# Performance work log

Hardware: AMD Instinct MI355X
Metric: run time of the kernel (lower is better)

## Reference

```python
import jax, jax.numpy as jnp
import numpy as np

B, T, D_ENC, H, NUM_CLASSES = 256, 256, 512, 512, 96


def setup_inputs() -> dict:
    key = jax.random.key(0)
    ks = jax.random.split(key, 12)
    s = lambda k, shp, fan: jax.random.normal(k, shp, jnp.float32) / np.sqrt(fan)
    return {
        "prev_h": jax.random.normal(ks[0], (B, H), jnp.float32),
        "prev_c": jax.random.normal(ks[1], (B, H), jnp.float32),
        "batch_H": jax.random.normal(ks[2], (B, T, D_ENC), jnp.float32),
        "char_onehots": jax.random.uniform(ks[3], (B, NUM_CLASSES), jnp.float32),
        # i2h: Dense(D_ENC -> H, no bias); h2h: Dense(H -> H, bias); score: Dense(H -> 1, no bias)
        "Wi2h": s(ks[4], (D_ENC, H), D_ENC),
        "Wh2h": s(ks[5], (H, H), H),
        "bh2h": jnp.zeros((H,), jnp.float32),
        "Wscore": s(ks[6], (H, 1), H),
        # LSTMCell: input dim = D_ENC + NUM_CLASSES, gates [i, f, g, o]
        "Wk": s(ks[7], (D_ENC + NUM_CLASSES, 4 * H), D_ENC + NUM_CLASSES),
        "Uk": s(ks[8], (H, 4 * H), H),
        "bk": jnp.zeros((4 * H,), jnp.float32),
    }


def reference(prev_h, prev_c, batch_H, char_onehots, Wi2h, Wh2h, bh2h, Wscore, Wk, Uk, bk):
    # Bahdanau additive attention
    bH_proj = jnp.einsum('btd,dh->bth', batch_H, Wi2h)          # [B,T,H]
    h_proj = (prev_h @ Wh2h + bh2h)[:, None, :]                  # [B,1,H]
    e = jnp.tanh(bH_proj + h_proj) @ Wscore                      # [B,T,1]
    alpha = jax.nn.softmax(e, axis=1)                            # [B,T,1]
    context = jnp.einsum('bt,btd->bd', alpha[..., 0], batch_H)   # [B,D_enc]
    # LSTM cell step on [context ; char_onehots]
    x = jnp.concatenate([context, char_onehots], axis=1)         # [B, D_enc+num_classes]
    z = x @ Wk + prev_h @ Uk + bk                                # [B, 4H]
    i, f, g, o = jnp.split(z, 4, axis=1)
    c_new = jax.nn.sigmoid(f) * prev_c + jax.nn.sigmoid(i) * jnp.tanh(g)
    h_new = jax.nn.sigmoid(o) * jnp.tanh(c_new)
    return h_new, c_new, alpha
```

## Files before the change

kernel.cpp:

```cpp
#include <hip/hip_runtime.h>

typedef __bf16 bf16_t;
typedef bf16_t bf16x8 __attribute__((ext_vector_type(8)));
typedef unsigned short ushort8_t __attribute__((ext_vector_type(8)));
typedef unsigned short ushort4_t __attribute__((ext_vector_type(4)));
typedef float f32x4 __attribute__((ext_vector_type(4)));

__device__ __forceinline__ unsigned short f2bf(float f) {
    __bf16 h = (__bf16)f;
    return __builtin_bit_cast(unsigned short, h);
}
__device__ __forceinline__ float fast_tanh(float x) {
    float e2 = __expf(2.f * x);
    return 1.f - 2.f / (e2 + 1.f);
}
__device__ __forceinline__ float fast_sig(float x) {
    return 1.f / (1.f + __expf(-x));
}

__global__ void k0_wt2(const float* __restrict__ Wi2h, const float* __restrict__ Wh2h,
                       unsigned short* __restrict__ Wt, unsigned short* __restrict__ Wht) {
    __shared__ float tile[32][33];
    const float* W = blockIdx.z ? Wh2h : Wi2h;
    unsigned short* O = blockIdx.z ? Wht : Wt;
    int tx = threadIdx.x, ty = threadIdx.y;
    int bx = blockIdx.x, by = blockIdx.y;
#pragma unroll
    for (int j = 0; j < 4; ++j) {
        int r = by * 32 + ty + j * 8;
        int c = bx * 32 + tx;
        tile[ty + j * 8][tx] = W[r * 512 + c];
    }
    __syncthreads();
#pragma unroll
    for (int j = 0; j < 4; ++j) {
        int h = bx * 32 + ty + j * 8;
        int d = by * 32 + tx;
        O[h * 512 + d] = f2bf(tile[tx][ty + j * 8]);
    }
}

__global__ void k1x_conv(const float* __restrict__ src, unsigned short* __restrict__ dst) {
    int i = blockIdx.x * 256 + threadIdx.x;
    float4 f = ((const float4*)src)[i];
    ushort4_t u;
    u[0] = f2bf(f.x); u[1] = f2bf(f.y); u[2] = f2bf(f.z); u[3] = f2bf(f.w);
    ((ushort4_t*)dst)[i] = u;
}

__global__ void k1m_hproj(const unsigned short* __restrict__ ph_bf,
                          const unsigned short* __restrict__ Wht,
                          const float* __restrict__ bh2h,
                          float* __restrict__ h_proj) {
    int tid = threadIdx.x;
    int wave = tid >> 6, lane = tid & 63;
    int l15 = lane & 15, g = lane >> 4;
    int h0 = blockIdx.x * 64 + wave * 16;
    int m0 = blockIdx.y * 32;

    f32x4 acc[2];
    acc[0] = (f32x4){0.f, 0.f, 0.f, 0.f};
    acc[1] = (f32x4){0.f, 0.f, 0.f, 0.f};

    const unsigned short* abase = ph_bf + (size_t)(m0 + l15) * 512 + g * 8;
    const unsigned short* bbase = Wht + (size_t)(h0 + l15) * 512 + g * 8;
#pragma unroll
    for (int j = 0; j < 16; ++j) {
        bf16x8 bf = __builtin_bit_cast(bf16x8, *(const ushort8_t*)(bbase + j * 32));
        bf16x8 a0 = __builtin_bit_cast(bf16x8, *(const ushort8_t*)(abase + j * 32));
        bf16x8 a1 = __builtin_bit_cast(bf16x8, *(const ushort8_t*)(abase + 16 * 512 + j * 32));
        acc[0] = __builtin_amdgcn_mfma_f32_16x16x32_bf16(a0, bf, acc[0], 0, 0, 0);
        acc[1] = __builtin_amdgcn_mfma_f32_16x16x32_bf16(a1, bf, acc[1], 0, 0, 0);
    }
    int h = h0 + l15;
    float bias = bh2h[h];
#pragma unroll
    for (int mf = 0; mf < 2; ++mf)
#pragma unroll
        for (int r = 0; r < 4; ++r)
            h_proj[(size_t)(m0 + mf * 16 + g * 4 + r) * 512 + h] = acc[mf][r] + bias;
}

__launch_bounds__(256, 1)
__global__ void k2v4_scores(const float* __restrict__ batch_H,
                            const unsigned short* __restrict__ Wt,
                            const float* __restrict__ h_proj,
                            const float* __restrict__ Wscore,
                            float* __restrict__ e_out) {
    __shared__ __align__(16) unsigned short Asw[128 * 512];
    __shared__ float hp_s[512];
    __shared__ float wsc_s[512];
    __shared__ float e_red[4][64];

    int tid = threadIdx.x;
    int m0  = blockIdx.x * 128;
    int b   = m0 >> 8;

    hp_s[tid]        = h_proj[(size_t)b * 512 + tid];
    hp_s[tid + 256]  = h_proj[(size_t)b * 512 + tid + 256];
    wsc_s[tid]       = Wscore[tid];
    wsc_s[tid + 256] = Wscore[tid + 256];

    {
        int dr = tid >> 4;
        int cc = tid & 15;
#pragma unroll
        for (int j = 0; j < 32; ++j) {
            int r = (j >> 2) * 16 + dr;
            int c = (j & 3) * 16 + cc;
            const float* src = batch_H + (size_t)(m0 + r) * 512 + c * 8;
            float4 f0 = *(const float4*)(src);
            float4 f1 = *(const float4*)(src + 4);
            ushort8_t u;
            u[0] = f2bf(f0.x); u[1] = f2bf(f0.y); u[2] = f2bf(f0.z); u[3] = f2bf(f0.w);
            u[4] = f2bf(f1.x); u[5] = f2bf(f1.y); u[6] = f2bf(f1.z); u[7] = f2bf(f1.w);
            *(ushort8_t*)((char*)Asw + r * 1024 + ((c ^ (r & 7)) << 4)) = u;
        }
    }
    __syncthreads();

    int wave = tid >> 6;
    int lane = tid & 63;
    int wr = wave >> 1;
    int wc = wave & 1;
    int l15 = lane & 15, g = lane >> 4;

    float s[4][4];
#pragma unroll
    for (int mf = 0; mf < 4; ++mf)
#pragma unroll
        for (int r = 0; r < 4; ++r) s[mf][r] = 0.f;

    const unsigned short* wtb = Wt + (size_t)(wc * 64 + l15) * 512 + g * 8;

    for (int nc = 0; nc < 4; ++nc) {
        f32x4 acc[4][4];
#pragma unroll
        for (int mf = 0; mf < 4; ++mf)
#pragma unroll
            for (int nf = 0; nf < 4; ++nf)
                acc[mf][nf] = (f32x4){0.f, 0.f, 0.f, 0.f};

        const unsigned short* wnc = wtb + (size_t)nc * 128 * 512;

        bf16x8 bq[4][4];
#pragma unroll
        for (int ks0 = 0; ks0 < 4; ++ks0)
#pragma unroll
            for (int nf = 0; nf < 4; ++nf)
                bq[ks0][nf] = __builtin_bit_cast(bf16x8,
                    *(const ushort8_t*)(wnc + (size_t)nf * 16 * 512 + ks0 * 32));

#pragma unroll
        for (int ks = 0; ks < 16; ++ks) {
            bf16x8 af[4];
#pragma unroll
            for (int mf = 0; mf < 4; ++mf) {
                int row = wr * 64 + mf * 16 + l15;
                af[mf] = __builtin_bit_cast(bf16x8,
                    *(const ushort8_t*)((char*)Asw + row * 1024 + (((ks * 4 + g) ^ (row & 7)) << 4)));
            }
#pragma unroll
            for (int nf = 0; nf < 4; ++nf)
#pragma unroll
                for (int mf = 0; mf < 4; ++mf)
                    acc[mf][nf] = __builtin_amdgcn_mfma_f32_16x16x32_bf16(
                        af[mf], bq[ks & 3][nf], acc[mf][nf], 0, 0, 0);
            if (ks < 12) {
#pragma unroll
                for (int nf = 0; nf < 4; ++nf)
                    bq[ks & 3][nf] = __builtin_bit_cast(bf16x8,
                        *(const ushort8_t*)(wnc + (size_t)nf * 16 * 512 + (ks + 4) * 32));
            }
        }

#pragma unroll
        for (int nf = 0; nf < 4; ++nf) {
            int nl = nc * 128 + wc * 64 + nf * 16 + l15;
            float hpv = hp_s[nl], wv = wsc_s[nl];
#pragma unroll
            for (int mf = 0; mf < 4; ++mf)
#pragma unroll
                for (int r = 0; r < 4; ++r)
                    s[mf][r] += wv * fast_tanh(acc[mf][nf][r] + hpv);
        }
    }

#pragma unroll
    for (int mf = 0; mf < 4; ++mf)
#pragma unroll
        for (int r = 0; r < 4; ++r) {
            float v = s[mf][r];
            v += __shfl_xor(v, 1);
            v += __shfl_xor(v, 2);
            v += __shfl_xor(v, 4);
            v += __shfl_xor(v, 8);
            s[mf][r] = v;
        }
    if (l15 == 0) {
#pragma unroll
        for (int mf = 0; mf < 4; ++mf)
#pragma unroll
            for (int r = 0; r < 4; ++r)
                e_red[wave][mf * 16 + g * 4 + r] = s[mf][r];
    }
    __syncthreads();
    if (tid < 128) {
        int wrr = tid >> 6, rl = tid & 63;
        e_out[m0 + wrr * 64 + rl] = e_red[wrr * 2 + 0][rl] + e_red[wrr * 2 + 1][rl];
    }
}

__global__ void k3_softmax(const float* __restrict__ e, float* __restrict__ alpha_out) {
    __shared__ float red[4];
    int b = blockIdx.x, tid = threadIdx.x;
    float v = e[b * 256 + tid];
    float mx = v;
#pragma unroll
    for (int off = 32; off; off >>= 1) mx = fmaxf(mx, __shfl_xor(mx, off));
    if ((tid & 63) == 0) red[tid >> 6] = mx;
    __syncthreads();
    mx = fmaxf(fmaxf(red[0], red[1]), fmaxf(red[2], red[3]));
    float p = __expf(v - mx);
    __syncthreads();
    float sum = p;
#pragma unroll
    for (int off = 32; off; off >>= 1) sum += __shfl_xor(sum, off);
    if ((tid & 63) == 0) red[tid >> 6] = sum;
    __syncthreads();
    sum = red[0] + red[1] + red[2] + red[3];
    alpha_out[b * 256 + tid] = p / sum;
}

__global__ void k4_context(const float* __restrict__ batch_H, const float* __restrict__ alpha,
                           float* __restrict__ context) {
    __shared__ float al[256];
    int b = blockIdx.y, dc = blockIdx.x, tid = threadIdx.x;
    al[tid] = alpha[b * 256 + tid];
    __syncthreads();
    int d = dc * 256 + tid;
    const float* bh = batch_H + (size_t)b * 256 * 512 + d;
    float acc = 0.f;
#pragma unroll 4
    for (int t = 0; t < 256; ++t)
        acc += al[t] * bh[(size_t)t * 512];
    context[b * 512 + d] = acc;
}

__global__ void k5t_wzt(const float* __restrict__ Wk, const float* __restrict__ Uk,
                        unsigned short* __restrict__ Wzt) {
    __shared__ float tile[32][33];
    int tx = threadIdx.x, ty = threadIdx.y;
    int bx = blockIdx.x;
    int by = blockIdx.y;
#pragma unroll
    for (int j = 0; j < 4; ++j) {
        int k = bx * 32 + ty + j * 8;
        int c = by * 32 + tx;
        float v = (k < 608) ? Wk[(size_t)k * 2048 + c] : Uk[(size_t)(k - 608) * 2048 + c];
        tile[ty + j * 8][tx] = v;
    }
    __syncthreads();
#pragma unroll
    for (int j = 0; j < 4; ++j) {
        int n = by * 32 + ty + j * 8;
        int k = bx * 32 + tx;
        Wzt[(size_t)n * 1120 + k] = f2bf(tile[tx][ty + j * 8]);
    }
}

__global__ void k5x_build(const float* __restrict__ context, const float* __restrict__ onehots,
                          const float* __restrict__ prev_h, unsigned short* __restrict__ xb) {
    int b = blockIdx.x, tid = threadIdx.x;
    for (int k = tid; k < 1120; k += 256) {
        float v;
        if (k < 512)      v = context[b * 512 + k];
        else if (k < 608) v = onehots[b * 96 + k - 512];
        else              v = prev_h[b * 512 + k - 608];
        xb[(size_t)b * 1120 + k] = f2bf(v);
    }
}

__launch_bounds__(256)
__global__ void k5m_fused(const unsigned short* __restrict__ xb,
                          const unsigned short* __restrict__ Wzt,
                          const float* __restrict__ bk,
                          const float* __restrict__ prev_c,
                          float* __restrict__ out) {
    __shared__ __align__(16) unsigned short Axs[32 * 232];

    int tid  = threadIdx.x;
    int wave = tid >> 6;
    int lane = tid & 63;
    int l15  = lane & 15;
    int g    = lane >> 4;
    int b0   = blockIdx.y * 32;
    int h0   = blockIdx.x * 64 + wave * 16;

    f32x4 acc[2][4];
#pragma unroll
    for (int mf = 0; mf < 2; ++mf)
#pragma unroll
        for (int gt = 0; gt < 4; ++gt)
            acc[mf][gt] = (f32x4){0.f, 0.f, 0.f, 0.f};

    const unsigned short* wbase = Wzt + (size_t)(h0 + l15) * 1120;

    for (int ks = 0; ks < 5; ++ks) {
        if (ks) __syncthreads();
        int kbase = ks * 224;
        for (int i = tid; i < 896; i += 256) {
            int row = i / 28;
            int c8  = (i % 28) * 8;
            *(ushort8_t*)(&Axs[row * 232 + c8]) =
                *(const ushort8_t*)(&xb[(size_t)(b0 + row) * 1120 + kbase + c8]);
        }
        __syncthreads();

        bf16x8 bcur[4], bnxt[4];
#pragma unroll
        for (int gt = 0; gt < 4; ++gt)
            bcur[gt] = __builtin_bit_cast(bf16x8,
                *(const ushort8_t*)(wbase + (size_t)gt * 512 * 1120 + kbase + g * 8));

#pragma unroll
        for (int kb = 0; kb < 7; ++kb) {
            if (kb < 6) {
                int kg = kbase + (kb + 1) * 32 + g * 8;
#pragma unroll
                for (int gt = 0; gt < 4; ++gt)
                    bnxt[gt] = __builtin_bit_cast(bf16x8,
                        *(const ushort8_t*)(wbase + (size_t)gt * 512 * 1120 + kg));
            }
            bf16x8 afrag[2];
#pragma unroll
            for (int mf = 0; mf < 2; ++mf)
                afrag[mf] = __builtin_bit_cast(bf16x8,
                    *(const ushort8_t*)(&Axs[(mf * 16 + l15) * 232 + kb * 32 + g * 8]));
#pragma unroll
            for (int gt = 0; gt < 4; ++gt)
#pragma unroll
                for (int mf = 0; mf < 2; ++mf)
                    acc[mf][gt] = __builtin_amdgcn_mfma_f32_16x16x32_bf16(
                        afrag[mf], bcur[gt], acc[mf][gt], 0, 0, 0);
#pragma unroll
            for (int gt = 0; gt < 4; ++gt) bcur[gt] = bnxt[gt];
        }
    }

    int h = h0 + l15;
    float bi = bk[h], bfv = bk[512 + h], bg = bk[1024 + h], bo = bk[1536 + h];
#pragma unroll
    for (int mf = 0; mf < 2; ++mf)
#pragma unroll
        for (int r = 0; r < 4; ++r) {
            int m = b0 + mf * 16 + g * 4 + r;
            float zi = acc[mf][0][r] + bi;
            float zf = acc[mf][1][r] + bfv;
            float zg = acc[mf][2][r] + bg;
            float zo = acc[mf][3][r] + bo;
            float c  = fast_sig(zf) * prev_c[m * 512 + h] + fast_sig(zi) * fast_tanh(zg);
            float hn = fast_sig(zo) * fast_tanh(c);
            out[m * 512 + h]          = hn;
            out[131072 + m * 512 + h] = c;
        }
}

extern "C" void kernel_launch(void* const* d_in, const int* in_sizes, int n_in,
                              void* d_out, int out_size, void* d_ws, size_t ws_size,
                              hipStream_t stream) {
    (void)in_sizes; (void)n_in; (void)out_size; (void)ws_size;
    const float* prev_h  = (const float*)d_in[0];
    const float* prev_c  = (const float*)d_in[1];
    const float* batch_H = (const float*)d_in[2];
    const float* onehots = (const float*)d_in[3];
    const float* Wi2h    = (const float*)d_in[4];
    const float* Wh2h    = (const float*)d_in[5];
    const float* bh2h    = (const float*)d_in[6];
    const float* Wscore  = (const float*)d_in[7];
    const float* Wk      = (const float*)d_in[8];
    const float* Uk      = (const float*)d_in[9];
    const float* bk      = (const float*)d_in[10];
    float* out = (float*)d_out;
    float* alpha = out + 262144;

    char* ws = (char*)d_ws;
    unsigned short* Wt     = (unsigned short*)(ws + 0);
    unsigned short* Wht    = (unsigned short*)(ws + 524288);
    unsigned short* ph_bf  = (unsigned short*)(ws + 1048576);
    float*          h_proj = (float*)(ws + 1310720);
    float*          e      = (float*)(ws + 1835008);
    unsigned short* Wzt    = (unsigned short*)(ws + 0);
    unsigned short* xb     = (unsigned short*)(ws + 4587520);
    float*          context= (float*)(ws + 5160960);

    k0_wt2     <<<dim3(16, 16, 2), dim3(32, 8), 0, stream>>>(Wi2h, Wh2h, Wt, Wht);
    k1x_conv   <<<128, 256, 0, stream>>>(prev_h, ph_bf);
    k1m_hproj  <<<dim3(8, 8), 256, 0, stream>>>(ph_bf, Wht, bh2h, h_proj);
    k2v4_scores<<<512, 256, 0, stream>>>(batch_H, Wt, h_proj, Wscore, e);
    k3_softmax <<<256, 256, 0, stream>>>(e, alpha);
    k4_context <<<dim3(2, 256), 256, 0, stream>>>(batch_H, alpha, context);
    k5t_wzt    <<<dim3(35, 64), dim3(32, 8), 0, stream>>>(Wk, Uk, Wzt);
    k5x_build  <<<256, 256, 0, stream>>>(context, onehots, prev_h, xb);
    k5m_fused  <<<dim3(8, 8), 256, 0, stream>>>(xb, Wzt, bk, prev_c, out);
}
```

Before: 177.5 us.

## Restructure attention scores kernel with LDS-resident weight tile and streamed activations

```diff
diff --git a/kernel.cpp b/kernel.cpp
--- a/kernel.cpp
+++ b/kernel.cpp
@@ -81,140 +81,155 @@
             h_proj[(size_t)(m0 + mf * 16 + g * 4 + r) * 512 + h] = acc[mf][r] + bias;
 }
 
-__launch_bounds__(256, 1)
-__global__ void k2v4_scores(const float* __restrict__ batch_H,
+__launch_bounds__(512, 1)
+__global__ void k2v5_scores(const float* __restrict__ batch_H,
                             const unsigned short* __restrict__ Wt,
                             const float* __restrict__ h_proj,
                             const float* __restrict__ Wscore,
-                            float* __restrict__ e_out) {
-    __shared__ __align__(16) unsigned short Asw[128 * 512];
-    __shared__ float hp_s[512];
-    __shared__ float wsc_s[512];
-    __shared__ float e_red[4][64];
-
-    int tid = threadIdx.x;
-    int m0  = blockIdx.x * 128;
-    int b   = m0 >> 8;
-
-    hp_s[tid]        = h_proj[(size_t)b * 512 + tid];
-    hp_s[tid + 256]  = h_proj[(size_t)b * 512 + tid + 256];
-    wsc_s[tid]       = Wscore[tid];
-    wsc_s[tid + 256] = Wscore[tid + 256];
-
-    {
-        int dr = tid >> 4;
-        int cc = tid & 15;
-#pragma unroll
-        for (int j = 0; j < 32; ++j) {
-            int r = (j >> 2) * 16 + dr;
-            int c = (j & 3) * 16 + cc;
-            const float* src = batch_H + (size_t)(m0 + r) * 512 + c * 8;
-            float4 f0 = *(const float4*)(src);
-            float4 f1 = *(const float4*)(src + 4);
-            ushort8_t u;
-            u[0] = f2bf(f0.x); u[1] = f2bf(f0.y); u[2] = f2bf(f0.z); u[3] = f2bf(f0.w);
-            u[4] = f2bf(f1.x); u[5] = f2bf(f1.y); u[6] = f2bf(f1.z); u[7] = f2bf(f1.w);
-            *(ushort8_t*)((char*)Asw + r * 1024 + ((c ^ (r & 7)) << 4)) = u;
-        }
-    }
-    __syncthreads();
-
+                            float* __restrict__ e_part8) {
+    __shared__ __align__(16) char Bsw[128 * 1024];
+
+    int tid  = threadIdx.x;
     int wave = tid >> 6;
     int lane = tid & 63;
-    int wr = wave >> 1;
-    int wc = wave & 1;
-    int l15 = lane & 15, g = lane >> 4;
-
-    float s[4][4];
-#pragma unroll
-    for (int mf = 0; mf < 4; ++mf)
-#pragma unroll
-        for (int r = 0; r < 4; ++r) s[mf][r] = 0.f;
-
-    const unsigned short* wtb = Wt + (size_t)(wc * 64 + l15) * 512 + g * 8;
-
-    for (int nc = 0; nc < 4; ++nc) {
-        f32x4 acc[4][4];
-#pragma unroll
-        for (int mf = 0; mf < 4; ++mf)
+    int l15  = lane & 15, g = lane >> 4;
+    int wr   = wave >> 1;
+    int wc   = wave & 1;
+
+    int xcd = blockIdx.x & 7, j = blockIdx.x >> 3;
+    int mgroup = xcd * 8 + (j >> 2);
+    int nt = j & 3;
+    int n0 = nt * 128;
+
+#pragma unroll
+    for (int i = 0; i < 16; ++i) {
+        int row = i * 8 + wave;
+        int chS = lane ^ (row & 7);
+        const unsigned short* src = Wt + (size_t)(n0 + row) * 512 + chS * 8;
+        __builtin_amdgcn_global_load_lds(
+            (const __attribute__((address_space(1))) void*)src,
+            (__attribute__((address_space(3))) void*)(Bsw + row * 1024), 16, 0, 0);
+    }
+    __syncthreads();
+
+    float wv[4];
+#pragma unroll
+    for (int nf = 0; nf < 4; ++nf)
+        wv[nf] = Wscore[n0 + wc * 64 + nf * 16 + l15];
+
+    int slot = nt * 2 + wc;
+
+    float4 pf[2][2][2];
+
+    {
+        int m00 = mgroup * 1024;
+#pragma unroll
+        for (int ks = 0; ks < 2; ++ks)
+#pragma unroll
+            for (int mf = 0; mf < 2; ++mf) {
+                const float* ap = batch_H + (size_t)(m00 + wr * 32 + mf * 16 + l15) * 512 + ks * 32 + g * 8;
+                pf[ks][mf][0] = *(const float4*)(ap);
+                pf[ks][mf][1] = *(const float4*)(ap + 4);
+            }
+    }
+
+    for (int p = 0; p < 8; ++p) {
+        int m0 = (mgroup * 8 + p) * 128;
+        int b  = (mgroup * 8 + p) >> 1;
+
+        float hp[4];
+#pragma unroll
+        for (int nf = 0; nf < 4; ++nf)
+            hp[nf] = h_proj[(size_t)b * 512 + n0 + wc * 64 + nf * 16 + l15];
+
+        f32x4 acc[2][4];
+#pragma unroll
+        for (int mf = 0; mf < 2; ++mf)
 #pragma unroll
             for (int nf = 0; nf < 4; ++nf)
                 acc[mf][nf] = (f32x4){0.f, 0.f, 0.f, 0.f};
 
-        const unsigned short* wnc = wtb + (size_t)nc * 128 * 512;
-
-        bf16x8 bq[4][4];
-#pragma unroll
-        for (int ks0 = 0; ks0 < 4; ++ks0)
-#pragma unroll
-            for (int nf = 0; nf < 4; ++nf)
-                bq[ks0][nf] = __builtin_bit_cast(bf16x8,
-                    *(const ushort8_t*)(wnc + (size_t)nf * 16 * 512 + ks0 * 32));
-
 #pragma unroll
         for (int ks = 0; ks < 16; ++ks) {
-            bf16x8 af[4];
-#pragma unroll
-            for (int mf = 0; mf < 4; ++mf) {
-                int row = wr * 64 + mf * 16 + l15;
-                af[mf] = __builtin_bit_cast(bf16x8,
-                    *(const ushort8_t*)((char*)Asw + row * 1024 + (((ks * 4 + g) ^ (row & 7)) << 4)));
-            }
-#pragma unroll
-            for (int nf = 0; nf < 4; ++nf)
-#pragma unroll
-                for (int mf = 0; mf < 4; ++mf)
+            const int par = ks & 1;
+            bf16x8 af[2];
+#pragma unroll
+            for (int mf = 0; mf < 2; ++mf) {
+                ushort8_t u;
+                u[0] = f2bf(pf[par][mf][0].x); u[1] = f2bf(pf[par][mf][0].y);
+                u[2] = f2bf(pf[par][mf][0].z); u[3] = f2bf(pf[par][mf][0].w);
+                u[4] = f2bf(pf[par][mf][1].x); u[5] = f2bf(pf[par][mf][1].y);
+                u[6] = f2bf(pf[par][mf][1].z); u[7] = f2bf(pf[par][mf][1].w);
+                af[mf] = __builtin_bit_cast(bf16x8, u);
+            }
+            if (ks < 14) {
+#pragma unroll
+                for (int mf = 0; mf < 2; ++mf) {
+                    const float* ap = batch_H + (size_t)(m0 + wr * 32 + mf * 16 + l15) * 512 + (ks + 2) * 32 + g * 8;
+                    pf[par][mf][0] = *(const float4*)(ap);
+                    pf[par][mf][1] = *(const float4*)(ap + 4);
+                }
+            } else if (p < 7) {
+#pragma unroll
+                for (int mf = 0; mf < 2; ++mf) {
+                    const float* ap = batch_H + (size_t)(m0 + 128 + wr * 32 + mf * 16 + l15) * 512 + (ks - 14) * 32 + g * 8;
+                    pf[par][mf][0] = *(const float4*)(ap);
+                    pf[par][mf][1] = *(const float4*)(ap + 4);
+                }
+            }
+#pragma unroll
+            for (int nf = 0; nf < 4; ++nf) {
+                int brow = wc * 64 + nf * 16 + l15;
+                bf16x8 bfv = __builtin_bit_cast(bf16x8,
+                    *(const ushort8_t*)(Bsw + brow * 1024 + (((ks * 4 + g) ^ (brow & 7)) << 4)));
+#pragma unroll
+                for (int mf = 0; mf < 2; ++mf)
                     acc[mf][nf] = __builtin_amdgcn_mfma_f32_16x16x32_bf16(
-                        af[mf], bq[ks & 3][nf], acc[mf][nf], 0, 0, 0);
-            if (ks < 12) {
-#pragma unroll
-                for (int nf = 0; nf < 4; ++nf)
-                    bq[ks & 3][nf] = __builtin_bit_cast(bf16x8,
-                        *(const ushort8_t*)(wnc + (size_t)nf * 16 * 512 + (ks + 4) * 32));
-            }
-        }
-
+                        af[mf], bfv, acc[mf][nf], 0, 0, 0);
+            }
+        }
+
+        float s[2][4];
+#pragma unroll
+        for (int mf = 0; mf < 2; ++mf)
+#pragma unroll
+            for (int r = 0; r < 4; ++r) s[mf][r] = 0.f;
 #pragma unroll
         for (int nf = 0; nf < 4; ++nf) {
-            int nl = nc * 128 + wc * 64 + nf * 16 + l15;
-            float hpv = hp_s[nl], wv = wsc_s[nl];
-#pragma unroll
-            for (int mf = 0; mf < 4; ++mf)
+#pragma unroll
+            for (int mf = 0; mf < 2; ++mf)
 #pragma unroll
                 for (int r = 0; r < 4; ++r)
-                    s[mf][r] += wv * fast_tanh(acc[mf][nf][r] + hpv);
-        }
-    }
-
-#pragma unroll
-    for (int mf = 0; mf < 4; ++mf)
-#pragma unroll
-        for (int r = 0; r < 4; ++r) {
-            float v = s[mf][r];
-            v += __shfl_xor(v, 1);
-            v += __shfl_xor(v, 2);
-            v += __shfl_xor(v, 4);
-            v += __shfl_xor(v, 8);
-            s[mf][r] = v;
-        }
-    if (l15 == 0) {
-#pragma unroll
-        for (int mf = 0; mf < 4; ++mf)
-#pragma unroll
-            for (int r = 0; r < 4; ++r)
-                e_red[wave][mf * 16 + g * 4 + r] = s[mf][r];
-    }
-    __syncthreads();
-    if (tid < 128) {
-        int wrr = tid >> 6, rl = tid & 63;
-        e_out[m0 + wrr * 64 + rl] = e_red[wrr * 2 + 0][rl] + e_red[wrr * 2 + 1][rl];
-    }
-}
-
-__global__ void k3_softmax(const float* __restrict__ e, float* __restrict__ alpha_out) {
+                    s[mf][r] += wv[nf] * fast_tanh(acc[mf][nf][r] + hp[nf]);
+        }
+#pragma unroll
+        for (int mf = 0; mf < 2; ++mf)
+#pragma unroll
+            for (int r = 0; r < 4; ++r) {
+                float v = s[mf][r];
+                v += __shfl_xor(v, 1);
+                v += __shfl_xor(v, 2);
+                v += __shfl_xor(v, 4);
+                v += __shfl_xor(v, 8);
+                s[mf][r] = v;
+            }
+        if (l15 == 0) {
+#pragma unroll
+            for (int mf = 0; mf < 2; ++mf) {
+                f32x4 o = (f32x4){s[mf][0], s[mf][1], s[mf][2], s[mf][3]};
+                *(f32x4*)(e_part8 + (size_t)slot * 65536 + m0 + wr * 32 + mf * 16 + g * 4) = o;
+            }
+        }
+    }
+}
+
+__global__ void k3_softmax(const float* __restrict__ e_part8, float* __restrict__ alpha_out) {
     __shared__ float red[4];
     int b = blockIdx.x, tid = threadIdx.x;
-    float v = e[b * 256 + tid];
+    int m = b * 256 + tid;
+    float v = 0.f;
+#pragma unroll
+    for (int s = 0; s < 8; ++s) v += e_part8[(size_t)s * 65536 + m];
     float mx = v;
 #pragma unroll
     for (int off = 32; off; off >>= 1) mx = fmaxf(mx, __shfl_xor(mx, off));
@@ -385,20 +400,20 @@
     float* alpha = out + 262144;
 
     char* ws = (char*)d_ws;
-    unsigned short* Wt     = (unsigned short*)(ws + 0);
-    unsigned short* Wht    = (unsigned short*)(ws + 524288);
-    unsigned short* ph_bf  = (unsigned short*)(ws + 1048576);
-    float*          h_proj = (float*)(ws + 1310720);
-    float*          e      = (float*)(ws + 1835008);
-    unsigned short* Wzt    = (unsigned short*)(ws + 0);
-    unsigned short* xb     = (unsigned short*)(ws + 4587520);
-    float*          context= (float*)(ws + 5160960);
+    unsigned short* Wt      = (unsigned short*)(ws + 0);
+    unsigned short* Wht     = (unsigned short*)(ws + 524288);
+    unsigned short* ph_bf   = (unsigned short*)(ws + 1048576);
+    float*          h_proj  = (float*)(ws + 1310720);
+    float*          e_part8 = (float*)(ws + 1835008);
+    unsigned short* Wzt     = (unsigned short*)(ws + 0);
+    unsigned short* xb      = (unsigned short*)(ws + 4587520);
+    float*          context = (float*)(ws + 5160960);
 
     k0_wt2     <<<dim3(16, 16, 2), dim3(32, 8), 0, stream>>>(Wi2h, Wh2h, Wt, Wht);
     k1x_conv   <<<128, 256, 0, stream>>>(prev_h, ph_bf);
     k1m_hproj  <<<dim3(8, 8), 256, 0, stream>>>(ph_bf, Wht, bh2h, h_proj);
-    k2v4_scores<<<512, 256, 0, stream>>>(batch_H, Wt, h_proj, Wscore, e);
-    k3_softmax <<<256, 256, 0, stream>>>(e, alpha);
+    k2v5_scores<<<256, 512, 0, stream>>>(batch_H, Wt, h_proj, Wscore, e_part8);
+    k3_softmax <<<256, 256, 0, stream>>>(e_part8, alpha);
     k4_context <<<dim3(2, 256), 256, 0, stream>>>(batch_H, alpha, context);
     k5t_wzt    <<<dim3(35, 64), dim3(32, 8), 0, stream>>>(Wk, Uk, Wzt);
     k5x_build  <<<256, 256, 0, stream>>>(context, onehots, prev_h, xb);
```

New measurement: 259.7 us. 1.46x slower.
